# Kernel optimization log

Measured on AMD Instinct MI355X. Metric: run time of the kernel, lower is better.

## Reference

```python
import jax, jax.numpy as jnp
import numpy as np

N_P, N_D, N_S = 100000, 1000, 5000      # patients, drugs, diseases
C, H, L = 64, 4, 2                       # hidden, heads, layers
DH = C // H                              # head dim
IN_P, IN_D, IN_S = 64, 128, 64           # raw feature dims per node type
E_PD, E_DP, E_DS, E_PS = 300000, 300000, 100000, 100000
EPS = 1e-16


def setup_inputs() -> dict:
    key = jax.random.key(0)
    ks = jax.random.split(key, 20)

    def lin(k, fin, fout, prefix=()):
        return jax.random.normal(k, prefix + (fin, fout), jnp.float32) / np.sqrt(fin).astype(np.float32)

    def edges(k, e, n_src, n_dst):
        k1, k2 = jax.random.split(k)
        return jnp.stack([jax.random.randint(k1, (e,), 0, n_src),
                          jax.random.randint(k2, (e,), 0, n_dst)]).astype(jnp.int32)

    inp = {}
    inp['x_p'] = jax.random.normal(ks[0], (N_P, IN_P), jnp.float32)
    inp['x_d'] = jax.random.normal(ks[1], (N_D, IN_D), jnp.float32)
    inp['x_s'] = jax.random.normal(ks[2], (N_S, IN_S), jnp.float32)
    inp['Win_p'] = lin(ks[3], IN_P, C); inp['bin_p'] = jnp.zeros((C,), jnp.float32)
    inp['Win_d'] = lin(ks[4], IN_D, C); inp['bin_d'] = jnp.zeros((C,), jnp.float32)
    inp['Win_s'] = lin(ks[5], IN_S, C); inp['bin_s'] = jnp.zeros((C,), jnp.float32)
    inp['Wk'] = lin(ks[6], C, C, (L, 3)); inp['bk'] = jnp.zeros((L, 3, C), jnp.float32)
    inp['Wq'] = lin(ks[7], C, C, (L, 3)); inp['bq'] = jnp.zeros((L, 3, C), jnp.float32)
    inp['Wv'] = lin(ks[8], C, C, (L, 3)); inp['bv'] = jnp.zeros((L, 3, C), jnp.float32)
    inp['Wa'] = lin(ks[9], C, C, (L, 3)); inp['ba'] = jnp.zeros((L, 3, C), jnp.float32)
    inp['a_rel'] = jax.random.normal(ks[10], (L, 4, H, DH, DH), jnp.float32) / np.sqrt(DH).astype(np.float32)
    inp['m_rel'] = jax.random.normal(ks[11], (L, 4, H, DH, DH), jnp.float32) / np.sqrt(DH).astype(np.float32)
    inp['p_rel'] = jnp.ones((L, 4, H), jnp.float32)   # PyG inits rel prior to ones
    inp['skip'] = jnp.ones((L, 3), jnp.float32)       # PyG inits skip gate to ones
    inp['ei_pd'] = edges(ks[12], E_PD, N_P, N_D)  # patient -takes-> drug
    inp['ei_dp'] = edges(ks[13], E_DP, N_D, N_P)  # drug -taken_by-> patient
    inp['ei_ds'] = edges(ks[14], E_DS, N_D, N_S)  # drug -treats-> disease
    inp['ei_ps'] = edges(ks[15], E_PS, N_P, N_S)  # patient -has-> disease
    return inp


def _hgt(x_p, x_d, x_s, Win_p, bin_p, Win_d, bin_d, Win_s, bin_s,
         Wk, bk, Wq, bq, Wv, bv, Wa, ba, a_rel, m_rel, p_rel, skip,
         ei_pd, ei_dp, ei_ds, ei_ps):
    Ns = (N_P, N_D, N_S)
    # per-node-type input projection (lin_dict)
    xs = [x_p @ Win_p + bin_p, x_d @ Win_d + bin_d, x_s @ Win_s + bin_s]
    # (src_type, dst_type, edge_index) for each relation
    edge_defs = [(0, 1, ei_pd), (1, 0, ei_dp), (1, 2, ei_ds), (0, 2, ei_ps)]
    inv_sqrt_d = np.float32(1.0 / np.sqrt(DH))

    for l in range(L):  # HGTConv layers
        k_t = [(xs[t] @ Wk[l, t] + bk[l, t]).reshape(Ns[t], H, DH) for t in range(3)]
        q_t = [(xs[t] @ Wq[l, t] + bq[l, t]).reshape(Ns[t], H, DH) for t in range(3)]
        v_t = [(xs[t] @ Wv[l, t] + bv[l, t]).reshape(Ns[t], H, DH) for t in range(3)]
        out = [jnp.zeros((Ns[t], H, DH), xs[t].dtype) for t in range(3)]
        for r, (st, dt, ei) in enumerate(edge_defs):
            src, dst = ei[0], ei[1]
            # relation-specific head-wise transforms of K and V
            k_rel = jnp.einsum('nhd,hde->nhe', k_t[st], a_rel[l, r])
            v_rel = jnp.einsum('nhd,hde->nhe', v_t[st], m_rel[l, r])
            # attention logits per edge, per head: [E, H]
            alpha = (q_t[dt][dst] * k_rel[src]).sum(-1) * (p_rel[l, r] * inv_sqrt_d)
            # segment softmax over incoming edges of each dst node (per relation)
            mx = jax.ops.segment_max(alpha, dst, num_segments=Ns[dt])
            a = jnp.exp(alpha - jax.lax.stop_gradient(mx)[dst])
            den = jax.ops.segment_sum(a, dst, num_segments=Ns[dt])
            a = a / (den[dst] + EPS)
            # attention-weighted scatter-add of messages, grouped by 'sum'
            out[dt] = out[dt] + jax.ops.segment_sum(v_rel[src] * a[:, :, None], dst, num_segments=Ns[dt])
        new_xs = []
        for t in range(3):
            o = jax.nn.gelu(out[t].reshape(Ns[t], C), approximate=False) @ Wa[l, t] + ba[l, t]
            s = jax.nn.sigmoid(skip[l, t])  # learned skip gate (in == out channels)
            new_xs.append(s * o + (1.0 - s) * xs[t])
        xs = new_xs
    # concatenate node-type outputs along node axis: [N_P+N_D+N_S, C]
    return jnp.concatenate(xs, axis=0)


def reference(x_p, x_d, x_s, Win_p, bin_p, Win_d, bin_d, Win_s, bin_s,
              Wk, bk, Wq, bq, Wv, bv, Wa, ba, a_rel, m_rel, p_rel, skip,
              ei_pd, ei_dp, ei_ds, ei_ps):
    return _hgt(x_p, x_d, x_s, Win_p, bin_p, Win_d, bin_d, Win_s, bin_s,
                Wk, bk, Wq, bq, Wv, bv, Wa, ba, a_rel, m_rel, p_rel, skip,
                ei_pd, ei_dp, ei_ds, ei_ps)
```

## Files before the change

kernel.cpp:

```cpp
#include <hip/hip_runtime.h>
#include <cmath>

typedef unsigned short ush;
typedef __attribute__((ext_vector_type(8))) short short8;
typedef __attribute__((ext_vector_type(4))) float floatx4;

static constexpr int N_P = 100000, N_D = 1000, N_S = 5000, NT = N_P + N_D + N_S;
static constexpr int NC = 111000;
static constexpr int E_TOT = 800000;

static constexpr int NB0 = 128, NB2 = 64, NB3 = 64;
static constexpr int CH0 = (300000 + NB0 - 1) / NB0;
static constexpr int CH2 = (100000 + NB2 - 1) / NB2;
static constexpr int HB0_OFF = 0;
static constexpr int HB2_OFF = NB0 * 1000;
static constexpr int HB3_OFF = HB2_OFF + NB2 * 5000;
static constexpr int NCH0 = NB0 / 16, NCH2 = NB2 / 16;
static constexpr int CS0_OFF = 0;
static constexpr int CS2_OFF = NCH0 * 1000;
static constexpr int CS3_OFF = CS2_OFF + NCH2 * 5000;
static constexpr int NHIST = NB0 + NB2 + NB3;
static constexpr int NBLK_R1 = (300000 + 255) / 256;
static constexpr int NZB = (100000 + 255) / 256;

__device__ __forceinline__ float b2f(ush b) { return __uint_as_float(((unsigned)b) << 16); }
__device__ __forceinline__ ush f2b(float f) {
    unsigned u = __float_as_uint(f);
    return (ush)((u + 0x7FFFu + ((u >> 16) & 1u)) >> 16);
}

__global__ __launch_bounds__(256) void detect_kernel(const ush* __restrict__ xp,
                                                     int* __restrict__ flag) {
    __shared__ int s;
    if (threadIdx.x == 0) s = 0;
    __syncthreads();
    int c = 0;
    for (int i = threadIdx.x; i < 16384; i += 256) {
        ush h = xp[i];
        if ((h & 0x7F80) == 0x7F80) c = 1;
    }
    if (c) atomicOr(&s, 1);
    __syncthreads();
    if (threadIdx.x == 0) *flag = s;
}

static constexpr size_t OFF_WINP = 0;
static constexpr size_t OFF_BINP = 4096;
static constexpr size_t OFF_WIND = 4160;
static constexpr size_t OFF_BIND = 12352;
static constexpr size_t OFF_WINS = 12416;
static constexpr size_t OFF_BINS = 16512;
static constexpr size_t OFF_WK = 16576;
static constexpr size_t OFF_BK = 41152;
static constexpr size_t OFF_WQ = 41536;
static constexpr size_t OFF_BQ = 66112;
static constexpr size_t OFF_WV = 66496;
static constexpr size_t OFF_BV = 91072;
static constexpr size_t OFF_WA = 91456;
static constexpr size_t OFF_BA = 116032;
static constexpr size_t OFF_AREL = 116416;
static constexpr size_t OFF_MREL = 124608;
static constexpr size_t OFF_PREL = 132800;
static constexpr size_t OFF_SKIP = 132832;
static constexpr size_t CW_TOTAL = 132838;
static constexpr int NCONVB = (int)((CW_TOTAL + 255) / 256);

struct ConvArgs {
    const void* src[18];
    long cum[19];
};

__global__ __launch_bounds__(256) void convert_kernel(ConvArgs a, ush* __restrict__ dst,
                                                      int* __restrict__ cnt_r1,
                                                      const int* __restrict__ flag) {
    const int b = blockIdx.x;
    if (b >= NCONVB) {
        int g = (b - NCONVB) * 256 + threadIdx.x;
        if (g < 100000) cnt_r1[g] = 0;
        return;
    }
    const int f = *flag;
    long g = (long)b * 256 + threadIdx.x;
    if (g >= (long)CW_TOTAL) return;
    int t = 0;
    while (g >= a.cum[t + 1]) t++;
    long i = g - a.cum[t];
    float v = f ? ((const float*)a.src[t])[i] : b2f(((const ush*)a.src[t])[i]);
    dst[g] = f2b(v);
}

struct CsrB {
    const int* ei[3];
    const int* ei1;
};

__device__ __forceinline__ void hist_geom(int b, const CsrB& c, int& r, const int*& ei, int& E,
                                          int& ndst, int& e0, int& e1, int& hb) {
    if (b < NB0) {
        r = 0; ei = c.ei[0]; E = 300000; ndst = 1000;
        e0 = b * CH0; hb = HB0_OFF + b * 1000;
    } else if (b < NB0 + NB2) {
        r = 1; ei = c.ei[1]; E = 100000; ndst = 5000;
        e0 = (b - NB0) * CH2; hb = HB2_OFF + (b - NB0) * 5000;
    } else {
        r = 2; ei = c.ei[2]; E = 100000; ndst = 5000;
        e0 = (b - NB0 - NB2) * CH2; hb = HB3_OFF + (b - NB0 - NB2) * 5000;
    }
    e1 = min(E, e0 + ((r == 0) ? CH0 : CH2));
}

__global__ __launch_bounds__(256) void count_kernel(CsrB c, int* __restrict__ HB,
                                                    int* __restrict__ cnt) {
    const int b = blockIdx.x;
    if (b >= NHIST) {
        int g = (b - NHIST) * 256 + threadIdx.x;
        if (g < 300000) atomicAdd(&cnt[1000 + c.ei1[300000 + g]], 1);
        return;
    }
    __shared__ int h[5000];
    int r, E, ndst, e0, e1, hb;
    const int* ei;
    hist_geom(b, c, r, ei, E, ndst, e0, e1, hb);
    for (int d = threadIdx.x; d < ndst; d += 256) h[d] = 0;
    __syncthreads();
    for (int e = e0 + threadIdx.x; e < e1; e += 256) atomicAdd(&h[ei[E + e]], 1);
    __syncthreads();
    for (int d = threadIdx.x; d < ndst; d += 256) HB[hb + d] = h[d];
}

__device__ __forceinline__ bool cs_geom(int g, int& idx0, int& step) {
    if (g >= 48000) return false;
    if (g < 8000) {
        int c = g / 1000, d = g % 1000;
        idx0 = HB0_OFF + c * 16 * 1000 + d; step = 1000;
    } else if (g < 28000) {
        int gg = g - 8000, c = gg / 5000, d = gg % 5000;
        idx0 = HB2_OFF + c * 16 * 5000 + d; step = 5000;
    } else {
        int gg = g - 28000, c = gg / 5000, d = gg % 5000;
        idx0 = HB3_OFF + c * 16 * 5000 + d; step = 5000;
    }
    return true;
}

__global__ __launch_bounds__(256) void sumHB_kernel(const int* __restrict__ HB,
                                                    int* __restrict__ CS) {
    int g = blockIdx.x * 256 + threadIdx.x;
    int idx0, step;
    if (!cs_geom(g, idx0, step)) return;
    int s = 0;
#pragma unroll
    for (int b = 0; b < 16; b++) s += HB[idx0 + b * step];
    CS[g] = s;
}

__global__ __launch_bounds__(256) void scanCS_kernel(int* __restrict__ CS,
                                                     int* __restrict__ cnt) {
    int d = blockIdx.x * 256 + threadIdx.x;
    if (d >= 11000) return;
    int ld, nch, cs0, step, roff;
    if (d < 1000) { ld = d; nch = NCH0; cs0 = CS0_OFF + ld; step = 1000; roff = 0; }
    else if (d < 6000) { ld = d - 1000; nch = NCH2; cs0 = CS2_OFF + ld; step = 5000; roff = 101000; }
    else { ld = d - 6000; nch = NCH2; cs0 = CS3_OFF + ld; step = 5000; roff = 106000; }
    int run = 0;
    for (int c = 0; c < nch; c++) {
        int t = CS[cs0 + c * step];
        CS[cs0 + c * step] = run;
        run += t;
    }
    cnt[roff + ld] = run;
}

__global__ __launch_bounds__(256) void fixHB_kernel(int* __restrict__ HB,
                                                    const int* __restrict__ CS) {
    int g = blockIdx.x * 256 + threadIdx.x;
    int idx0, step;
    if (!cs_geom(g, idx0, step)) return;
    int run = CS[g];
#pragma unroll
    for (int b = 0; b < 16; b++) {
        int t = HB[idx0 + b * step];
        HB[idx0 + b * step] = run;
        run += t;
    }
}

__global__ __launch_bounds__(256) void scanA_kernel(const int* __restrict__ cnt,
                                                    int* __restrict__ tmp,
                                                    int* __restrict__ part) {
    __shared__ int ls[256];
    const int t = threadIdx.x;
    const int base = blockIdx.x * 1024 + t * 4;
    int v[4];
#pragma unroll
    for (int j = 0; j < 4; j++) v[j] = (base + j < NC) ? cnt[base + j] : 0;
    int tsum = v[0] + v[1] + v[2] + v[3];
    ls[t] = tsum;
    __syncthreads();
    for (int off = 1; off < 256; off <<= 1) {
        int y = (t >= off) ? ls[t - off] : 0;
        __syncthreads();
        ls[t] += y;
        __syncthreads();
    }
    int run = ls[t] - tsum;
#pragma unroll
    for (int j = 0; j < 4; j++) {
        if (base + j < NC) tmp[base + j] = run;
        run += v[j];
    }
    if (t == 255) part[blockIdx.x] = ls[255];
}

__global__ __launch_bounds__(256) void scanB_kernel(int* __restrict__ part, int nb) {
    __shared__ int ls[256];
    const int t = threadIdx.x;
    int x = (t < nb) ? part[t] : 0;
    ls[t] = x;
    __syncthreads();
    for (int off = 1; off < 256; off <<= 1) {
        int y = (t >= off) ? ls[t - off] : 0;
        __syncthreads();
        ls[t] += y;
        __syncthreads();
    }
    if (t < nb) part[t] = ls[t] - x;
    if (t == nb - 1) part[nb] = ls[t];
}

static constexpr int NSCB = (NC + 1 + 255) / 256;
__global__ __launch_bounds__(256) void scanC_kernel(const int* __restrict__ tmp,
                                                    const int* __restrict__ part,
                                                    int* __restrict__ rowptr,
                                                    int* __restrict__ cnt_r1) {
    const int b = blockIdx.x;
    if (b >= NSCB) {
        int g = (b - NSCB) * 256 + threadIdx.x;
        if (g < 100000) cnt_r1[g] = 0;
        return;
    }
    int i = b * 256 + threadIdx.x;
    if (i > NC) return;
    rowptr[i] = (i == NC) ? part[(NC + 1023) / 1024] : tmp[i] + part[i >> 10];
}

__global__ __launch_bounds__(256) void fill_kernel(CsrB c, const int* __restrict__ HB,
                                                   const int* __restrict__ rowptr,
                                                   int* __restrict__ fillpos,
                                                   int* __restrict__ col) {
    const int b = blockIdx.x;
    if (b >= NHIST) {
        int g = (b - NHIST) * 256 + threadIdx.x;
        if (g < 300000) {
            int gi = 1000 + c.ei1[300000 + g];
            int slot = rowptr[gi] + atomicAdd(&fillpos[gi], 1);
            col[slot] = c.ei1[g];
        }
        return;
    }
    __shared__ int h[5000];
    int r, E, ndst, e0, e1, hb;
    const int* ei;
    hist_geom(b, c, r, ei, E, ndst, e0, e1, hb);
    const int roff = (r == 0) ? 0 : (r == 1) ? 101000 : 106000;
    for (int d = threadIdx.x; d < ndst; d += 256) h[d] = rowptr[roff + d] + HB[hb + d];
    __syncthreads();
    for (int e = e0 + threadIdx.x; e < e1; e += 256) {
        int d = ei[E + e];
        int slot = atomicAdd(&h[d], 1);
        col[slot] = ei[e];
    }
}

__global__ __launch_bounds__(256) void eff_kernel(const ush* __restrict__ CW,
                                                  ush* __restrict__ weff) {
    const int b = blockIdx.x;
    const int l = b >> 2, r = b & 3;
    const int st_of[4] = {0, 1, 1, 0};
    const int st = st_of[r];
    ush* out = weff + (size_t)b * 8320;
    for (int idx = threadIdx.x; idx < 8320; idx += 256) {
        int n, k;
        if (idx < 8192) { k = idx >> 7; n = idx & 127; }
        else { k = -1; n = idx - 8192; }
        int kv = n >= 64;
        int j = n & 63, h = j >> 4, e = j & 15;
        const ush* W = CW + (kv ? OFF_WV : OFF_WK) + (size_t)(l * 3 + st) * 4096;
        const ush* B = CW + (kv ? OFF_BV : OFF_BK) + (size_t)(l * 3 + st) * 64;
        const ush* R = CW + (kv ? OFF_MREL : OFF_AREL) + (size_t)(l * 4 + r) * 1024;
        float acc = 0.f;
        if (k >= 0) {
#pragma unroll
            for (int d = 0; d < 16; d++)
                acc += b2f(W[k * 64 + h * 16 + d]) * b2f(R[h * 256 + d * 16 + e]);
        } else {
#pragma unroll
            for (int d = 0; d < 16; d++)
                acc += b2f(B[h * 16 + d]) * b2f(R[h * 256 + d * 16 + e]);
        }
        out[idx] = f2b(acc);
    }
}

template <int K>
__device__ __forceinline__ void stage_A(short* sA, const ush* __restrict__ X, int M, int row0) {
    for (int cid = threadIdx.x; cid < 64 * K / 8; cid += 256) {
        int r = cid / (K / 8), c0 = (cid % (K / 8)) * 8;
        int row = row0 + r;
        short8 v = {0, 0, 0, 0, 0, 0, 0, 0};
        if (row < M) v = *(const short8*)(const void*)(X + (size_t)row * K + c0);
        *(short8*)(&sA[r * (K + 8) + c0]) = v;
    }
}

template <int K>
__device__ __forceinline__ void stage_A_raw(short* sA, const void* __restrict__ X, int f,
                                            int M, int row0) {
    for (int cid = threadIdx.x; cid < 64 * K / 8; cid += 256) {
        int r = cid / (K / 8), c0 = (cid % (K / 8)) * 8;
        int row = row0 + r;
        short8 v = {0, 0, 0, 0, 0, 0, 0, 0};
        if (row < M) {
            if (f) {
// ... 32 lines not shown
#pragma unroll
    for (int c = 0; c < NOUT / 16; c++) {
        float bv = b2f(Bb[16 * c + (l & 15)]);
        acc[c] = (floatx4){bv, bv, bv, bv};
    }
#pragma unroll
    for (int s = 0; s < K / 32; s++) {
        short8 a = *(const short8*)(&sA[(16 * w + (l & 15)) * (K + 8) + 32 * s + ((l >> 4) << 3)]);
#pragma unroll
        for (int c = 0; c < NOUT / 16; c++) {
            short8 b = *(const short8*)(&sB[(s * (NOUT / 16) + c) * 512 + l * 8]);
            acc[c] = __builtin_amdgcn_mfma_f32_16x16x32_bf16(a, b, acc[c], 0, 0, 0);
        }
    }
#pragma unroll
    for (int c = 0; c < NOUT / 16; c++)
#pragma unroll
        for (int r = 0; r < 4; r++) {
            int row = row0 + 16 * w + ((l >> 4) << 2) + r;
            if (row < M) Y[(size_t)row * NOUT + 16 * c + (l & 15)] = f2b(acc[c][r]);
        }
}

struct InArgs {
    const void* raw[3];
    const ush* W[3];
    const ush* Bb[3];
    ush* X;
    const int* flag;
};

__global__ __launch_bounds__(256) void inproj_kernel(InArgs a) {
    extern __shared__ short smem[];
    const int b = blockIdx.x;
    const int f = *a.flag;
    if (b < 1563) {
        short* sA = smem;
        short* sB = smem + 64 * 72;
        stage_A_raw<64>(sA, a.raw[0], f, N_P, b * 64);
        gemm_core<64, 64>(sA, sB, a.W[0], a.Bb[0], a.X, N_P, b * 64);
    } else if (b < 1579) {
        short* sA = smem;
        short* sB = smem + 64 * 136;
        stage_A_raw<128>(sA, a.raw[1], f, N_D, (b - 1563) * 64);
        gemm_core<128, 64>(sA, sB, a.W[1], a.Bb[1], a.X + (size_t)N_P * 64, N_D,
                           (b - 1563) * 64);
    } else {
        short* sA = smem;
        short* sB = smem + 64 * 72;
        stage_A_raw<64>(sA, a.raw[2], f, N_S, (b - 1579) * 64);
        gemm_core<64, 64>(sA, sB, a.W[2], a.Bb[2], a.X + (size_t)(N_P + N_D) * 64, N_S,
                          (b - 1579) * 64);
    }
}

struct QKVArgs {
    const ush* X;
    ush* Q;
    const ush* Wq[3];
    const ush* Bq[3];
    const ush* Xr[4];
    ush* Y[4];
    const ush* Wkv[4];
    const ush* Bkv[4];
};

__global__ __launch_bounds__(256) void qkv_kernel(QKVArgs a) {
    extern __shared__ short smem[];
    short* sA = smem;
    short* sB = smem + 64 * 72;
    const int b = blockIdx.x;
    if (b < 1658) {
        int t, lb, M;
        size_t noff;
        if (b < 1563) { t = 0; lb = b; M = N_P; noff = 0; }
        else if (b < 1579) { t = 1; lb = b - 1563; M = N_D; noff = (size_t)N_P; }
        else { t = 2; lb = b - 1579; M = N_S; noff = (size_t)(N_P + N_D); }
        stage_A<64>(sA, a.X + noff * 64, M, lb * 64);
        gemm_core<64, 64>(sA, sB, a.Wq[t], a.Bq[t], a.Q + noff * 64, M, lb * 64);
    } else {
        int bb = b - 1658;
        int r, lb, M;
        if (bb < 1563) { r = 0; lb = bb; M = N_P; }
        else if (bb < 1579) { r = 1; lb = bb - 1563; M = N_D; }
        else if (bb < 1595) { r = 2; lb = bb - 1579; M = N_D; }
        else { r = 3; lb = bb - 1595; M = N_P; }
        stage_A<64>(sA, a.Xr[r], M, lb * 64);
        gemm_core<64, 128>(sA, sB, a.Wkv[r], a.Bkv[r], a.Y[r], M, lb * 64);
    }
}

struct AggrArgs {
    const int* rowptr;
    const int* col;
    const ush* KV[4];
    const ush* Q;
    const ush* prel;
    float* OUT;
};

template <int LANES>
__device__ __forceinline__ void seg_attn(const AggrArgs& a, int rel, int g, int h, int lane,
                                         const float* qf, float* o) {
    const int s0 = a.rowptr[g], s1 = a.rowptr[g + 1];
    const ush* KV = a.KV[rel];
    const float ps = b2f(a.prel[rel * 4 + h]) * 0.25f;
    float m = -1e30f, s = 0.f;
    float acc[16];
#pragma unroll
    for (int i = 0; i < 16; i++) acc[i] = 0.f;
    for (int j = s0 + lane; j < s1; j += LANES) {
        int src = a.col[j];
        const ush* kp = KV + (size_t)src * 128 + h * 16;
        short8 k0 = *(const short8*)(const void*)kp;
        short8 k1 = *(const short8*)(const void*)(kp + 8);
        short8 v0 = *(const short8*)(const void*)(kp + 64);
        short8 v1 = *(const short8*)(const void*)(kp + 72);
        float dot = 0.f;
#pragma unroll
        for (int i = 0; i < 8; i++) dot += qf[i] * b2f((ush)k0[i]);
#pragma unroll
// ... 26 lines not shown
#pragma unroll
    for (int i = 0; i < 16; i++) o[i] += acc[i] * inv;
}

template <int LANES>
__device__ __forceinline__ void job_run(const AggrArgs& a, int wid, int nd, int rel, int roff,
                                        size_t xoff, int rel2, int roff2) {
    const int lane = wid % LANES;
    const int grp = wid / LANES;
    const int d = grp >> 2, h = grp & 3;
    if (d >= nd) return;
    const ush* qp = a.Q + xoff + (size_t)d * 64 + h * 16;
    short8 q0 = *(const short8*)(const void*)qp;
    short8 q1 = *(const short8*)(const void*)(qp + 8);
    float qf[16];
#pragma unroll
    for (int i = 0; i < 8; i++) { qf[i] = b2f((ush)q0[i]); qf[8 + i] = b2f((ush)q1[i]); }
    float o[16];
#pragma unroll
    for (int i = 0; i < 16; i++) o[i] = 0.f;
    seg_attn<LANES>(a, rel, roff + d, h, lane, qf, o);
    if (rel2 >= 0) seg_attn<LANES>(a, rel2, roff2 + d, h, lane, qf, o);
    if (lane == 0) {
        float* op = a.OUT + xoff + (size_t)d * 64 + h * 16;
#pragma unroll
        for (int i = 0; i < 4; i++)
            *(floatx4*)(op + 4 * i) =
                (floatx4){o[4 * i], o[4 * i + 1], o[4 * i + 2], o[4 * i + 3]};
    }
}

__global__ __launch_bounds__(256) void aggr_kernel(AggrArgs a) {
    const int b = blockIdx.x, t = threadIdx.x;
    if (b < 250) {
        job_run<16>(a, b * 256 + t, N_D, 0, 0, (size_t)N_P * 64, -1, 0);
    } else if (b < 563) {
        job_run<4>(a, (b - 250) * 256 + t, N_S, 2, 101000, (size_t)(N_P + N_D) * 64, 3, 106000);
    } else {
        job_run<2>(a, (b - 563) * 256 + t, N_P, 1, 1000, 0, -1, 0);
    }
}

struct EpiArgs {
    const float* O;
    ush* X;
    const ush* W[3];
    const ush* Bb[3];
    const ush* skipv;
    void* fout;
    const int* flag;
    int last;
};

__global__ __launch_bounds__(256) void epi_kernel(EpiArgs a) {
    const int b = blockIdx.x;
    int t, lb, M;
    size_t noff;
    if (b < 1563) { t = 0; lb = b; M = N_P; noff = 0; }
    else if (b < 1579) { t = 1; lb = b - 1563; M = N_D; noff = (size_t)N_P; }
    else { t = 2; lb = b - 1579; M = N_S; noff = (size_t)(N_P + N_D); }
    const float* O = a.O + noff * 64;
    ush* X = a.X + noff * 64;
    const ush* W = a.W[t];
    __shared__ short sA[64 * 72];
    __shared__ short sB[8 * 512];
    const int tid = threadIdx.x;
    const int row0 = lb * 64;
    for (int cid = tid; cid < 512; cid += 256) {
        int r = cid >> 3, c0 = (cid & 7) * 8;
        int row = row0 + r;
        short8 sv = {0, 0, 0, 0, 0, 0, 0, 0};
        if (row < M) {
#pragma unroll
            for (int j = 0; j < 8; j++) {
                float v = O[(size_t)row * 64 + c0 + j];
                sv[j] = (short)f2b(0.5f * v * (1.0f + erff(v * 0.70710678118654752f)));
            }
        }
        *(short8*)(&sA[r * 72 + c0]) = sv;
    }
    __syncthreads();
    const float sg = 1.f / (1.f + expf(-b2f(a.skipv[t])));
    for (int u = tid; u < 512; u += 256) {
        int f = u >> 6, l = u & 63;
        int s = f >> 2, c = f & 3;
        int kbase = 32 * s + ((l >> 4) << 3), n = 16 * c + (l & 15);
        short8 v;
#pragma unroll
        for (int j = 0; j < 8; j++) v[j] = (short)W[(size_t)(kbase + j) * 64 + n];
        *(short8*)(&sB[f * 512 + l * 8]) = v;
    }
    __syncthreads();
    const int w = tid >> 6, l = tid & 63;
    floatx4 acc[4];
#pragma unroll
    for (int c = 0; c < 4; c++) {
        float bv = b2f(a.Bb[t][16 * c + (l & 15)]);
        acc[c] = (floatx4){bv, bv, bv, bv};
    }
#pragma unroll
    for (int s = 0; s < 2; s++) {
        short8 av = *(const short8*)(&sA[(16 * w + (l & 15)) * 72 + 32 * s + ((l >> 4) << 3)]);
#pragma unroll
        for (int c = 0; c < 4; c++) {
            short8 bv = *(const short8*)(&sB[(s * 4 + c) * 512 + l * 8]);
            acc[c] = __builtin_amdgcn_mfma_f32_16x16x32_bf16(av, bv, acc[c], 0, 0, 0);
        }
    }
    const int fl = a.last ? *a.flag : 0;
#pragma unroll
    for (int c = 0; c < 4; c++)
#pragma unroll
        for (int r = 0; r < 4; r++) {
            int row = row0 + 16 * w + ((l >> 4) << 2) + r;
            if (row >= M) continue;
            size_t off = (size_t)row * 64 + 16 * c + (l & 15);
            float val = sg * acc[c][r] + (1.f - sg) * b2f(X[off]);
            if (!a.last) {
                X[off] = f2b(val);
            } else {
                size_t goff = (noff + row) * 64 + 16 * c + (l & 15);
                if (fl)
                    ((float*)a.fout)[goff] = val;
                else
                    ((ush*)a.fout)[goff] = f2b(val);
            }
        }
}

extern "C" void kernel_launch(void* const* d_in, const int* in_sizes, int n_in,
                              void* d_out, int out_size, void* d_ws, size_t ws_size,
                              hipStream_t stream) {
    char* w = (char*)d_ws;
    int* FLAG = (int*)w;    w += 64;
    ush* CW = (ush*)w;      w += ((CW_TOTAL * 2 + 63) / 64) * 64;
    ush* WEFFB = (ush*)w;   w += ((size_t)8 * 8320 * 2 + 63) / 64 * 64;
    ush* X = (ush*)w;       w += (size_t)NT * 64 * 2;
    ush* Q = (ush*)w;       w += (size_t)NT * 64 * 2;
    ush* KV0 = (ush*)w;     w += (size_t)N_P * 128 * 2;
    ush* KV1 = (ush*)w;     w += (size_t)N_D * 128 * 2;
    ush* KV2 = (ush*)w;     w += (size_t)N_D * 128 * 2;
    ush* KV3 = (ush*)w;     w += (size_t)N_P * 128 * 2;
    float* OUT = (float*)w; w += (size_t)NT * 64 * 4;
    int* CNT = (int*)w;     w += (size_t)NC * 4;
    int* TMP = (int*)w;     w += (size_t)NC * 4;
    int* PART = (int*)w;    w += 512;
    int* ROWPTR = (int*)w;  w += (size_t)(NC + 1) * 4;
    int* COL = (int*)w;     w += (size_t)E_TOT * 4;
    int* HB = (int*)OUT;
    int* CS = (int*)OUT + 800000;

    detect_kernel<<<1, 256, 0, stream>>>((const ush*)d_in[0], FLAG);
    static const long sz[18] = {4096, 64, 8192, 64, 4096, 64, 24576, 384, 24576, 384,
                                24576, 384, 24576, 384, 8192, 8192, 32, 6};
    ConvArgs ca;
    long cum = 0;
    for (int t = 0; t < 18; t++) {
        ca.src[t] = d_in[3 + t];
        ca.cum[t] = cum;
        cum += sz[t];
    }
    ca.cum[18] = cum;
    convert_kernel<<<NCONVB + NZB, 256, 0, stream>>>(ca, CW, CNT + 1000, FLAG);

    CsrB cb;
    cb.ei[0] = (const int*)d_in[21];
    cb.ei[1] = (const int*)d_in[23];
    cb.ei[2] = (const int*)d_in[24];
    cb.ei1 = (const int*)d_in[22];
    count_kernel<<<NHIST + NBLK_R1, 256, 0, stream>>>(cb, HB, CNT);
    sumHB_kernel<<<(48000 + 255) / 256, 256, 0, stream>>>(HB, CS);
    scanCS_kernel<<<(11000 + 255) / 256, 256, 0, stream>>>(CS, CNT);
    scanA_kernel<<<(NC + 1023) / 1024, 256, 0, stream>>>(CNT, TMP, PART);
    scanB_kernel<<<1, 256, 0, stream>>>(PART, (NC + 1023) / 1024);
    scanC_kernel<<<NSCB + NZB, 256, 0, stream>>>(TMP, PART, ROWPTR, CNT + 1000);
    fixHB_kernel<<<(48000 + 255) / 256, 256, 0, stream>>>(HB, CS);
    fill_kernel<<<NHIST + NBLK_R1, 256, 0, stream>>>(cb, HB, ROWPTR, CNT, COL);

    eff_kernel<<<8, 256, 0, stream>>>(CW, WEFFB);

    const size_t toff[3] = {0, (size_t)N_P, (size_t)(N_P + N_D)};

    InArgs ia;
    ia.raw[0] = d_in[0];
    ia.raw[1] = d_in[1];
    ia.raw[2] = d_in[2];
    ia.W[0] = CW + OFF_WINP; ia.Bb[0] = CW + OFF_BINP;
    ia.W[1] = CW + OFF_WIND; ia.Bb[1] = CW + OFF_BIND;
    ia.W[2] = CW + OFF_WINS; ia.Bb[2] = CW + OFF_BINS;
    ia.X = X;
    ia.flag = FLAG;
    inproj_kernel<<<1658, 256, 33792, stream>>>(ia);

    for (int l = 0; l < 2; l++) {
        QKVArgs qk;
        qk.X = X;
        qk.Q = Q;
        ush* KVr[4] = {KV0, KV1, KV2, KV3};
        const int rst[4] = {0, 1, 1, 0};
        for (int t = 0; t < 3; t++) {
            qk.Wq[t] = CW + OFF_WQ + (size_t)(l * 3 + t) * 4096;
            qk.Bq[t] = CW + OFF_BQ + (l * 3 + t) * 64;
        }
        for (int r = 0; r < 4; r++) {
            qk.Xr[r] = X + toff[rst[r]] * 64;
            qk.Y[r] = KVr[r];
            const ush* we = WEFFB + (size_t)(l * 4 + r) * 8320;
            qk.Wkv[r] = we;
            qk.Bkv[r] = we + 8192;
        }
        qkv_kernel<<<4816, 256, 25600, stream>>>(qk);

        AggrArgs aa;
        aa.rowptr = ROWPTR;
        aa.col = COL;
        for (int r = 0; r < 4; r++) aa.KV[r] = KVr[r];
        aa.Q = Q;
        aa.prel = CW + OFF_PREL + l * 16;
        aa.OUT = OUT;
        aggr_kernel<<<3688, 256, 0, stream>>>(aa);

        EpiArgs ea;
        ea.O = OUT;
        ea.X = X;
        for (int t = 0; t < 3; t++) {
            ea.W[t] = CW + OFF_WA + (size_t)(l * 3 + t) * 4096;
            ea.Bb[t] = CW + OFF_BA + (l * 3 + t) * 64;
        }
        ea.skipv = CW + OFF_SKIP + l * 3;
        ea.fout = d_out;
        ea.flag = FLAG;
        ea.last = (l == 1) ? 1 : 0;
        epi_kernel<<<1658, 256, 0, stream>>>(ea);
    }
}
```

Measured before the change: 393.6 us.

## Fuse CSR build, projections and QKV into fewer launches; apply GELU in aggregation

Collapses the many small CSR-construction, scan, weight-conversion and projection kernels into four combined launches, and overlaps CSR fill with the first-layer QKV GEMM. QKV now reads each node tile once and produces Q plus both relation K/V outputs from it. GELU moves from the epilogue into the aggregation store, so the intermediate is written as bf16 instead of fp32. The runtime dtype-detect kernel is replaced by host-side checks on input sizes. The main costs targeted are launch overhead, repeated activation reads and intermediate traffic; the price is larger shared memory per block and more branching inside the merged kernels.

```diff
diff --git a/kernel.cpp b/kernel.cpp
--- a/kernel.cpp
+++ b/kernel.cpp
@@ -27,21 +27,6 @@
 __device__ __forceinline__ ush f2b(float f) {
     unsigned u = __float_as_uint(f);
     return (ush)((u + 0x7FFFu + ((u >> 16) & 1u)) >> 16);
-}
-
-__global__ __launch_bounds__(256) void detect_kernel(const ush* __restrict__ xp,
-                                                     int* __restrict__ flag) {
-    __shared__ int s;
-    if (threadIdx.x == 0) s = 0;
-    __syncthreads();
-    int c = 0;
-    for (int i = threadIdx.x; i < 16384; i += 256) {
-        ush h = xp[i];
-        if ((h & 0x7F80) == 0x7F80) c = 1;
-    }
-    if (c) atomicOr(&s, 1);
-    __syncthreads();
-    if (threadIdx.x == 0) *flag = s;
 }
 
 static constexpr size_t OFF_WINP = 0;
@@ -64,30 +49,13 @@
 static constexpr size_t OFF_SKIP = 132832;
 static constexpr size_t CW_TOTAL = 132838;
 static constexpr int NCONVB = (int)((CW_TOTAL + 255) / 256);
+static constexpr int NSCB = (NC + 1 + 255) / 256;
 
 struct ConvArgs {
     const void* src[18];
     long cum[19];
+    int fl[18];
 };
-
-__global__ __launch_bounds__(256) void convert_kernel(ConvArgs a, ush* __restrict__ dst,
-                                                      int* __restrict__ cnt_r1,
-                                                      const int* __restrict__ flag) {
-    const int b = blockIdx.x;
-    if (b >= NCONVB) {
-        int g = (b - NCONVB) * 256 + threadIdx.x;
-        if (g < 100000) cnt_r1[g] = 0;
-        return;
-    }
-    const int f = *flag;
-    long g = (long)b * 256 + threadIdx.x;
-    if (g >= (long)CW_TOTAL) return;
-    int t = 0;
-    while (g >= a.cum[t + 1]) t++;
-    long i = g - a.cum[t];
-    float v = f ? ((const float*)a.src[t])[i] : b2f(((const ush*)a.src[t])[i]);
-    dst[g] = f2b(v);
-}
 
 struct CsrB {
     const int* ei[3];
@@ -109,25 +77,6 @@
     e1 = min(E, e0 + ((r == 0) ? CH0 : CH2));
 }
 
-__global__ __launch_bounds__(256) void count_kernel(CsrB c, int* __restrict__ HB,
-                                                    int* __restrict__ cnt) {
-    const int b = blockIdx.x;
-    if (b >= NHIST) {
-        int g = (b - NHIST) * 256 + threadIdx.x;
-        if (g < 300000) atomicAdd(&cnt[1000 + c.ei1[300000 + g]], 1);
-        return;
-    }
-    __shared__ int h[5000];
-    int r, E, ndst, e0, e1, hb;
-    const int* ei;
-    hist_geom(b, c, r, ei, E, ndst, e0, e1, hb);
-    for (int d = threadIdx.x; d < ndst; d += 256) h[d] = 0;
-    __syncthreads();
-    for (int e = e0 + threadIdx.x; e < e1; e += 256) atomicAdd(&h[ei[E + e]], 1);
-    __syncthreads();
-    for (int d = threadIdx.x; d < ndst; d += 256) HB[hb + d] = h[d];
-}
-
 __device__ __forceinline__ bool cs_geom(int g, int& idx0, int& step) {
     if (g >= 48000) return false;
     if (g < 8000) {
@@ -143,162 +92,31 @@
     return true;
 }
 
-__global__ __launch_bounds__(256) void sumHB_kernel(const int* __restrict__ HB,
-                                                    int* __restrict__ CS) {
-    int g = blockIdx.x * 256 + threadIdx.x;
-    int idx0, step;
-    if (!cs_geom(g, idx0, step)) return;
-    int s = 0;
-#pragma unroll
-    for (int b = 0; b < 16; b++) s += HB[idx0 + b * step];
-    CS[g] = s;
-}
-
-__global__ __launch_bounds__(256) void scanCS_kernel(int* __restrict__ CS,
-                                                     int* __restrict__ cnt) {
-    int d = blockIdx.x * 256 + threadIdx.x;
-    if (d >= 11000) return;
-    int ld, nch, cs0, step, roff;
-    if (d < 1000) { ld = d; nch = NCH0; cs0 = CS0_OFF + ld; step = 1000; roff = 0; }
-    else if (d < 6000) { ld = d - 1000; nch = NCH2; cs0 = CS2_OFF + ld; step = 5000; roff = 101000; }
-    else { ld = d - 6000; nch = NCH2; cs0 = CS3_OFF + ld; step = 5000; roff = 106000; }
-    int run = 0;
-    for (int c = 0; c < nch; c++) {
-        int t = CS[cs0 + c * step];
-        CS[cs0 + c * step] = run;
-        run += t;
-    }
-    cnt[roff + ld] = run;
-}
-
-__global__ __launch_bounds__(256) void fixHB_kernel(int* __restrict__ HB,
-                                                    const int* __restrict__ CS) {
-    int g = blockIdx.x * 256 + threadIdx.x;
-    int idx0, step;
-    if (!cs_geom(g, idx0, step)) return;
-    int run = CS[g];
-#pragma unroll
-    for (int b = 0; b < 16; b++) {
-        int t = HB[idx0 + b * step];
-        HB[idx0 + b * step] = run;
-        run += t;
-    }
-}
-
-__global__ __launch_bounds__(256) void scanA_kernel(const int* __restrict__ cnt,
-                                                    int* __restrict__ tmp,
-                                                    int* __restrict__ part) {
-    __shared__ int ls[256];
-    const int t = threadIdx.x;
-    const int base = blockIdx.x * 1024 + t * 4;
-    int v[4];
-#pragma unroll
-    for (int j = 0; j < 4; j++) v[j] = (base + j < NC) ? cnt[base + j] : 0;
-    int tsum = v[0] + v[1] + v[2] + v[3];
-    ls[t] = tsum;
-    __syncthreads();
-    for (int off = 1; off < 256; off <<= 1) {
-        int y = (t >= off) ? ls[t - off] : 0;
+__global__ __launch_bounds__(256) void k1_kernel(ConvArgs a, ush* __restrict__ dst,
+                                                 int* __restrict__ cnt_r1, CsrB c,
+                                                 int* __restrict__ HB) {
+    const int b = blockIdx.x;
+    if (b < NCONVB) {
+        long g = (long)b * 256 + threadIdx.x;
+        if (g >= (long)CW_TOTAL) return;
+        int t = 0;
+        while (g >= a.cum[t + 1]) t++;
+        long i = g - a.cum[t];
+        float v = a.fl[t] ? ((const float*)a.src[t])[i] : b2f(((const ush*)a.src[t])[i]);
+        dst[g] = f2b(v);
+    } else if (b < NCONVB + NZB) {
+        int g = (b - NCONVB) * 256 + threadIdx.x;
+        if (g < 100000) cnt_r1[g] = 0;
+    } else {
+        __shared__ int h[5000];
+        int r, E, ndst, e0, e1, hb;
+        const int* ei;
+        hist_geom(b - NCONVB - NZB, c, r, ei, E, ndst, e0, e1, hb);
+        for (int d = threadIdx.x; d < ndst; d += 256) h[d] = 0;
         __syncthreads();
-        ls[t] += y;
+        for (int e = e0 + threadIdx.x; e < e1; e += 256) atomicAdd(&h[ei[E + e]], 1);
         __syncthreads();
-    }
-    int run = ls[t] - tsum;
-#pragma unroll
-    for (int j = 0; j < 4; j++) {
-        if (base + j < NC) tmp[base + j] = run;
-        run += v[j];
-    }
-    if (t == 255) part[blockIdx.x] = ls[255];
-}
-
-__global__ __launch_bounds__(256) void scanB_kernel(int* __restrict__ part, int nb) {
-    __shared__ int ls[256];
-    const int t = threadIdx.x;
-    int x = (t < nb) ? part[t] : 0;
-    ls[t] = x;
-    __syncthreads();
-    for (int off = 1; off < 256; off <<= 1) {
-        int y = (t >= off) ? ls[t - off] : 0;
-        __syncthreads();
-        ls[t] += y;
-        __syncthreads();
-    }
-    if (t < nb) part[t] = ls[t] - x;
-    if (t == nb - 1) part[nb] = ls[t];
-}
-
-static constexpr int NSCB = (NC + 1 + 255) / 256;
-__global__ __launch_bounds__(256) void scanC_kernel(const int* __restrict__ tmp,
-                                                    const int* __restrict__ part,
-                                                    int* __restrict__ rowptr,
-                                                    int* __restrict__ cnt_r1) {
-    const int b = blockIdx.x;
-    if (b >= NSCB) {
-        int g = (b - NSCB) * 256 + threadIdx.x;
-        if (g < 100000) cnt_r1[g] = 0;
-        return;
-    }
-    int i = b * 256 + threadIdx.x;
-    if (i > NC) return;
-    rowptr[i] = (i == NC) ? part[(NC + 1023) / 1024] : tmp[i] + part[i >> 10];
-}
-
-__global__ __launch_bounds__(256) void fill_kernel(CsrB c, const int* __restrict__ HB,
-                                                   const int* __restrict__ rowptr,
-                                                   int* __restrict__ fillpos,
-                                                   int* __restrict__ col) {
-    const int b = blockIdx.x;
-    if (b >= NHIST) {
-        int g = (b - NHIST) * 256 + threadIdx.x;
-        if (g < 300000) {
-            int gi = 1000 + c.ei1[300000 + g];
-            int slot = rowptr[gi] + atomicAdd(&fillpos[gi], 1);
-            col[slot] = c.ei1[g];
-        }
-        return;
-    }
-    __shared__ int h[5000];
-    int r, E, ndst, e0, e1, hb;
-    const int* ei;
-    hist_geom(b, c, r, ei, E, ndst, e0, e1, hb);
-    const int roff = (r == 0) ? 0 : (r == 1) ? 101000 : 106000;
-    for (int d = threadIdx.x; d < ndst; d += 256) h[d] = rowptr[roff + d] + HB[hb + d];
-    __syncthreads();
-    for (int e = e0 + threadIdx.x; e < e1; e += 256) {
-        int d = ei[E + e];
-        int slot = atomicAdd(&h[d], 1);
-        col[slot] = ei[e];
-    }
-}
-
-__global__ __launch_bounds__(256) void eff_kernel(const ush* __restrict__ CW,
-                                                  ush* __restrict__ weff) {
-    const int b = blockIdx.x;
-    const int l = b >> 2, r = b & 3;
-    const int st_of[4] = {0, 1, 1, 0};
-    const int st = st_of[r];
-    ush* out = weff + (size_t)b * 8320;
-    for (int idx = threadIdx.x; idx < 8320; idx += 256) {
-        int n, k;
-        if (idx < 8192) { k = idx >> 7; n = idx & 127; }
-        else { k = -1; n = idx - 8192; }
-        int kv = n >= 64;
-        int j = n & 63, h = j >> 4, e = j & 15;
-        const ush* W = CW + (kv ? OFF_WV : OFF_WK) + (size_t)(l * 3 + st) * 4096;
-        const ush* B = CW + (kv ? OFF_BV : OFF_BK) + (size_t)(l * 3 + st) * 64;
-        const ush* R = CW + (kv ? OFF_MREL : OFF_AREL) + (size_t)(l * 4 + r) * 1024;
-        float acc = 0.f;
-        if (k >= 0) {
-#pragma unroll
-            for (int d = 0; d < 16; d++)
-                acc += b2f(W[k * 64 + h * 16 + d]) * b2f(R[h * 256 + d * 16 + e]);
-        } else {
-#pragma unroll
-            for (int d = 0; d < 16; d++)
-                acc += b2f(B[h * 16 + d]) * b2f(R[h * 256 + d * 16 + e]);
-        }
-        out[idx] = f2b(acc);
+        for (int d = threadIdx.x; d < ndst; d += 256) HB[hb + d] = h[d];
     }
 }
 
@@ -377,71 +195,270 @@
         }
 }
 
-struct InArgs {
+template <int NG>
+__device__ __forceinline__ void gemm_wide(const short* sA, short* sB,
+                                          const ush* __restrict__ Wq, const ush* __restrict__ Bq,
+                                          ush* __restrict__ Yq,
+                                          const ush* __restrict__ WeA, ush* __restrict__ YA,
+                                          const ush* __restrict__ WeB, ush* __restrict__ YB,
+                                          int M, int row0) {
+    constexpr int NF = 2 * NG;
+    const int tid = threadIdx.x;
+    for (int u = tid; u < NF * 64; u += 256) {
+        int f = u >> 6, l = u & 63;
+        int s = f / NG, c = f % NG;
+        int kbase = 32 * s + ((l >> 4) << 3);
+        const ush* W; int ld, cw;
+        if (c < 4) { W = Wq; ld = 64; cw = 16 * c; }
+        else if (c < 12) { W = WeA; ld = 128; cw = 16 * (c - 4); }
+        else { W = WeB; ld = 128; cw = 16 * (c - 12); }
+        int n = cw + (l & 15);
+        short8 v;
+#pragma unroll
+        for (int j = 0; j < 8; j++) v[j] = (short)W[(size_t)(kbase + j) * ld + n];
+        *(short8*)(&sB[f * 512 + l * 8]) = v;
+    }
+    __syncthreads();
+    const int w = tid >> 6, l = tid & 63;
+    floatx4 acc[NG];
+#pragma unroll
+    for (int c = 0; c < NG; c++) {
+        float bv;
+        if (c < 4) bv = b2f(Bq[16 * c + (l & 15)]);
+        else if (c < 12) bv = b2f(WeA[8192 + 16 * (c - 4) + (l & 15)]);
+        else bv = b2f(WeB[8192 + 16 * (c - 12) + (l & 15)]);
+        acc[c] = (floatx4){bv, bv, bv, bv};
+    }
+#pragma unroll
+    for (int s = 0; s < 2; s++) {
+        short8 a = *(const short8*)(&sA[(16 * w + (l & 15)) * 72 + 32 * s + ((l >> 4) << 3)]);
+#pragma unroll
+        for (int c = 0; c < NG; c++) {
+            short8 b = *(const short8*)(&sB[(s * NG + c) * 512 + l * 8]);
+            acc[c] = __builtin_amdgcn_mfma_f32_16x16x32_bf16(a, b, acc[c], 0, 0, 0);
+        }
+    }
+#pragma unroll
+    for (int c = 0; c < NG; c++)
+#pragma unroll
+        for (int r = 0; r < 4; r++) {
+            int row = row0 + 16 * w + ((l >> 4) << 2) + r;
+            if (row >= M) continue;
+            ush val = f2b(acc[c][r]);
+            if (c < 4) Yq[(size_t)row * 64 + 16 * c + (l & 15)] = val;
+            else if (c < 12) YA[(size_t)row * 128 + 16 * (c - 4) + (l & 15)] = val;
+            else YB[(size_t)row * 128 + 16 * (c - 12) + (l & 15)] = val;
+        }
+}
+
+struct K2Args {
     const void* raw[3];
+    int f[3];
     const ush* W[3];
     const ush* Bb[3];
     ush* X;
-    const int* flag;
+    const int* HB;
+    int* CS;
+    int* cnt;
+    const int* ei1;
 };
 
-__global__ __launch_bounds__(256) void inproj_kernel(InArgs a) {
+__global__ __launch_bounds__(256) void k2_kernel(K2Args a) {
     extern __shared__ short smem[];
     const int b = blockIdx.x;
-    const int f = *a.flag;
-    if (b < 1563) {
-        short* sA = smem;
-        short* sB = smem + 64 * 72;
-        stage_A_raw<64>(sA, a.raw[0], f, N_P, b * 64);
-        gemm_core<64, 64>(sA, sB, a.W[0], a.Bb[0], a.X, N_P, b * 64);
-    } else if (b < 1579) {
-        short* sA = smem;
-        short* sB = smem + 64 * 136;
-        stage_A_raw<128>(sA, a.raw[1], f, N_D, (b - 1563) * 64);
-        gemm_core<128, 64>(sA, sB, a.W[1], a.Bb[1], a.X + (size_t)N_P * 64, N_D,
-                           (b - 1563) * 64);
+    if (b < 1658) {
+        if (b < 1563) {
+            short* sA = smem; short* sB = smem + 64 * 72;
+            stage_A_raw<64>(sA, a.raw[0], a.f[0], N_P, b * 64);
+            gemm_core<64, 64>(sA, sB, a.W[0], a.Bb[0], a.X, N_P, b * 64);
+        } else if (b < 1579) {
+            short* sA = smem; short* sB = smem + 64 * 136;
+            stage_A_raw<128>(sA, a.raw[1], a.f[1], N_D, (b - 1563) * 64);
+            gemm_core<128, 64>(sA, sB, a.W[1], a.Bb[1], a.X + (size_t)N_P * 64, N_D,
+                               (b - 1563) * 64);
+        } else {
+            short* sA = smem; short* sB = smem + 64 * 72;
+            stage_A_raw<64>(sA, a.raw[2], a.f[2], N_S, (b - 1579) * 64);
+            gemm_core<64, 64>(sA, sB, a.W[2], a.Bb[2], a.X + (size_t)(N_P + N_D) * 64, N_S,
+                              (b - 1579) * 64);
+        }
+    } else if (b < 1701) {
+        int d = (b - 1658) * 256 + threadIdx.x;
+        if (d >= 11000) return;
+        int ld_, nch, base, step, cs0, csstep, roff;
+        if (d < 1000) { ld_ = d; nch = NCH0; base = HB0_OFF + ld_; step = 1000;
+                        cs0 = CS0_OFF + ld_; csstep = 1000; roff = 0; }
+        else if (d < 6000) { ld_ = d - 1000; nch = NCH2; base = HB2_OFF + ld_; step = 5000;
+                             cs0 = CS2_OFF + ld_; csstep = 5000; roff = 101000; }
+        else { ld_ = d - 6000; nch = NCH2; base = HB3_OFF + ld_; step = 5000;
+               cs0 = CS3_OFF + ld_; csstep = 5000; roff = 106000; }
+        int run = 0;
+        for (int cc = 0; cc < nch; cc++) {
+            int s = 0;
+#pragma unroll
+            for (int bb = 0; bb < 16; bb++) s += a.HB[base + (cc * 16 + bb) * step];
+            a.CS[cs0 + cc * csstep] = run;
+            run += s;
+        }
+        a.cnt[roff + ld_] = run;
     } else {
-        short* sA = smem;
-        short* sB = smem + 64 * 72;
-        stage_A_raw<64>(sA, a.raw[2], f, N_S, (b - 1579) * 64);
-        gemm_core<64, 64>(sA, sB, a.W[2], a.Bb[2], a.X + (size_t)(N_P + N_D) * 64, N_S,
-                          (b - 1579) * 64);
+        int g = (b - 1701) * 256 + threadIdx.x;
+        if (g < 300000) atomicAdd(&a.cnt[1000 + a.ei1[300000 + g]], 1);
+    }
+}
+
+__global__ __launch_bounds__(256) void k3_kernel(const int* __restrict__ cnt,
+                                                 int* __restrict__ tmp,
+                                                 int* __restrict__ part,
+                                                 const ush* __restrict__ CW,
+                                                 ush* __restrict__ weff) {
+    const int b = blockIdx.x;
+    if (b < 109) {
+        __shared__ int ls[256];
+        const int t = threadIdx.x;
+        const int base = b * 1024 + t * 4;
+        int v[4];
+#pragma unroll
+        for (int j = 0; j < 4; j++) v[j] = (base + j < NC) ? cnt[base + j] : 0;
+        int tsum = v[0] + v[1] + v[2] + v[3];
+        ls[t] = tsum;
+        __syncthreads();
+        for (int off = 1; off < 256; off <<= 1) {
+            int y = (t >= off) ? ls[t - off] : 0;
+            __syncthreads();
+            ls[t] += y;
+            __syncthreads();
+        }
+        int run = ls[t] - tsum;
+#pragma unroll
+        for (int j = 0; j < 4; j++) {
+            if (base + j < NC) tmp[base + j] = run;
+            run += v[j];
+        }
+        if (t == 255) part[b] = ls[255];
+    } else {
+        const int eb = b - 109;
+        const int l = eb >> 2, r = eb & 3;
+        const int st_of[4] = {0, 1, 1, 0};
+        const int st = st_of[r];
+        ush* out = weff + (size_t)eb * 8320;
+        for (int idx = threadIdx.x; idx < 8320; idx += 256) {
+            int n, k;
+            if (idx < 8192) { k = idx >> 7; n = idx & 127; }
+            else { k = -1; n = idx - 8192; }
+            int kv = n >= 64;
+            int j = n & 63, h = j >> 4, e = j & 15;
+            const ush* W = CW + (kv ? OFF_WV : OFF_WK) + (size_t)(l * 3 + st) * 4096;
+            const ush* B = CW + (kv ? OFF_BV : OFF_BK) + (size_t)(l * 3 + st) * 64;
+            const ush* R = CW + (kv ? OFF_MREL : OFF_AREL) + (size_t)(l * 4 + r) * 1024;
+            float acc = 0.f;
+            if (k >= 0) {
+#pragma unroll
+                for (int d = 0; d < 16; d++)
+                    acc += b2f(W[k * 64 + h * 16 + d]) * b2f(R[h * 256 + d * 16 + e]);
+            } else {
+#pragma unroll
+                for (int d = 0; d < 16; d++)
+                    acc += b2f(B[h * 16 + d]) * b2f(R[h * 256 + d * 16 + e]);
+            }
+            out[idx] = f2b(acc);
+        }
+    }
+}
+
+__global__ __launch_bounds__(256) void k4_kernel(const int* __restrict__ tmp,
+                                                 const int* __restrict__ part,
+                                                 int* __restrict__ rowptr,
+                                                 int* __restrict__ HB,
+                                                 const int* __restrict__ CS,
+                                                 int* __restrict__ fillpos) {
+    const int b = blockIdx.x;
+    if (b < NSCB) {
+        __shared__ int ls[256];
+        const int t = threadIdx.x;
+        ls[t] = (t < 109) ? part[t] : 0;
+        __syncthreads();
+        for (int off = 1; off < 256; off <<= 1) {
+            int y = (t >= off) ? ls[t - off] : 0;
+            __syncthreads();
+            ls[t] += y;
+            __syncthreads();
+        }
+        int i = b * 256 + t;
+        if (i <= NC)
+            rowptr[i] = (i == NC) ? ls[255] : tmp[i] + ((i >> 10) ? ls[(i >> 10) - 1] : 0);
+    } else if (b < NSCB + 188) {
+        int g = (b - NSCB) * 256 + threadIdx.x;
+        int idx0, step;
+        if (!cs_geom(g, idx0, step)) return;
+        int run = CS[g];
+#pragma unroll
+        for (int bb = 0; bb < 16; bb++) {
+            int t2 = HB[idx0 + bb * step];
+            HB[idx0 + bb * step] = run;
+            run += t2;
+        }
+    } else {
+        int g = (b - NSCB - 188) * 256 + threadIdx.x;
+        if (g < 100000) fillpos[g] = 0;
     }
 }
 
 struct QKVArgs {
     const ush* X;
     ush* Q;
+    ush* KV[4];
     const ush* Wq[3];
     const ush* Bq[3];
-    const ush* Xr[4];
-    ush* Y[4];
-    const ush* Wkv[4];
-    const ush* Bkv[4];
+    const ush* We[4];
+    CsrB cb;
+    const int* HB;
+    const int* rowptr;
+    int* fillpos;
+    int* col;
 };
 
-__global__ __launch_bounds__(256) void qkv_kernel(QKVArgs a) {
+__global__ __launch_bounds__(256) void qkvfill_kernel(QKVArgs a) {
     extern __shared__ short smem[];
-    short* sA = smem;
-    short* sB = smem + 64 * 72;
     const int b = blockIdx.x;
     if (b < 1658) {
-        int t, lb, M;
-        size_t noff;
-        if (b < 1563) { t = 0; lb = b; M = N_P; noff = 0; }
-        else if (b < 1579) { t = 1; lb = b - 1563; M = N_D; noff = (size_t)N_P; }
-        else { t = 2; lb = b - 1579; M = N_S; noff = (size_t)(N_P + N_D); }
-        stage_A<64>(sA, a.X + noff * 64, M, lb * 64);
-        gemm_core<64, 64>(sA, sB, a.Wq[t], a.Bq[t], a.Q + noff * 64, M, lb * 64);
+        short* sA = smem;
+        short* sB = smem + 64 * 72;
+        if (b < 1563) {
+            stage_A<64>(sA, a.X, N_P, b * 64);
+            gemm_wide<20>(sA, sB, a.Wq[0], a.Bq[0], a.Q, a.We[0], a.KV[0], a.We[3], a.KV[3],
+                          N_P, b * 64);
+        } else if (b < 1579) {
+            int lb = b - 1563;
+            stage_A<64>(sA, a.X + (size_t)N_P * 64, N_D, lb * 64);
+            gemm_wide<20>(sA, sB, a.Wq[1], a.Bq[1], a.Q + (size_t)N_P * 64, a.We[1], a.KV[1],
+                          a.We[2], a.KV[2], N_D, lb * 64);
+        } else {
+            int lb = b - 1579;
+            stage_A<64>(sA, a.X + (size_t)(N_P + N_D) * 64, N_S, lb * 64);
+            gemm_wide<4>(sA, sB, a.Wq[2], a.Bq[2], a.Q + (size_t)(N_P + N_D) * 64,
+                         nullptr, nullptr, nullptr, nullptr, N_S, lb * 64);
+        }
+    } else if (b < 1658 + NHIST) {
+        int* h = (int*)smem;
+        int r, E, ndst, e0, e1, hb;
+        const int* ei;
+        hist_geom(b - 1658, a.cb, r, ei, E, ndst, e0, e1, hb);
+        const int roff = (r == 0) ? 0 : (r == 1) ? 101000 : 106000;
+        for (int d = threadIdx.x; d < ndst; d += 256) h[d] = a.rowptr[roff + d] + a.HB[hb + d];
+        __syncthreads();
+        for (int e = e0 + threadIdx.x; e < e1; e += 256) {
+            int d = ei[E + e];
+            int slot = atomicAdd(&h[d], 1);
+            a.col[slot] = ei[e];
+        }
     } else {
-        int bb = b - 1658;
-        int r, lb, M;
-        if (bb < 1563) { r = 0; lb = bb; M = N_P; }
-        else if (bb < 1579) { r = 1; lb = bb - 1563; M = N_D; }
-        else if (bb < 1595) { r = 2; lb = bb - 1579; M = N_D; }
-        else { r = 3; lb = bb - 1595; M = N_P; }
-        stage_A<64>(sA, a.Xr[r], M, lb * 64);
-        gemm_core<64, 128>(sA, sB, a.Wkv[r], a.Bkv[r], a.Y[r], M, lb * 64);
+        int g = (b - 1658 - NHIST) * 256 + threadIdx.x;
+        if (g < 300000) {
+            int gi = 1000 + a.cb.ei1[300000 + g];
+            int slot = a.rowptr[gi] + atomicAdd(&a.fillpos[gi], 1);
+            a.col[slot] = a.cb.ei1[g];
+        }
     }
 }
 
@@ -451,7 +468,7 @@
     const ush* KV[4];
     const ush* Q;
     const ush* prel;
-    float* OUT;
+    ush* OUT;
 };
 
 template <int LANES>
@@ -524,11 +541,17 @@
     seg_attn<LANES>(a, rel, roff + d, h, lane, qf, o);
     if (rel2 >= 0) seg_attn<LANES>(a, rel2, roff2 + d, h, lane, qf, o);
     if (lane == 0) {
-        float* op = a.OUT + xoff + (size_t)d * 64 + h * 16;
-#pragma unroll
-        for (int i = 0; i < 4; i++)
-            *(floatx4*)(op + 4 * i) =
-                (floatx4){o[4 * i], o[4 * i + 1], o[4 * i + 2], o[4 * i + 3]};
+        ush* op = a.OUT + xoff + (size_t)d * 64 + h * 16;
+        short8 w0, w1;
+#pragma unroll
+        for (int i = 0; i < 8; i++) {
+            float va = o[i];
+            w0[i] = (short)f2b(0.5f * va * (1.0f + erff(va * 0.70710678118654752f)));
+            float vb = o[8 + i];
+            w1[i] = (short)f2b(0.5f * vb * (1.0f + erff(vb * 0.70710678118654752f)));
+        }
+        *(short8*)(op) = w0;
+        *(short8*)(op + 8) = w1;
     }
 }
 
@@ -544,13 +567,13 @@
 }
 
 struct EpiArgs {
-    const float* O;
+    const ush* O;
     ush* X;
     const ush* W[3];
     const ush* Bb[3];
     const ush* skipv;
     void* fout;
-    const int* flag;
+    int foutf;
     int last;
 };
 
@@ -561,7 +584,7 @@
     if (b < 1563) { t = 0; lb = b; M = N_P; noff = 0; }
     else if (b < 1579) { t = 1; lb = b - 1563; M = N_D; noff = (size_t)N_P; }
     else { t = 2; lb = b - 1579; M = N_S; noff = (size_t)(N_P + N_D); }
-    const float* O = a.O + noff * 64;
+    const ush* O = a.O + noff * 64;
     ush* X = a.X + noff * 64;
     const ush* W = a.W[t];
     __shared__ short sA[64 * 72];
@@ -572,13 +595,7 @@
         int r = cid >> 3, c0 = (cid & 7) * 8;
         int row = row0 + r;
         short8 sv = {0, 0, 0, 0, 0, 0, 0, 0};
-        if (row < M) {
-#pragma unroll
-            for (int j = 0; j < 8; j++) {
-                float v = O[(size_t)row * 64 + c0 + j];
-                sv[j] = (short)f2b(0.5f * v * (1.0f + erff(v * 0.70710678118654752f)));
-            }
-        }
+        if (row < M) sv = *(const short8*)(const void*)(O + (size_t)row * 64 + c0);
         *(short8*)(&sA[r * 72 + c0]) = sv;
     }
     __syncthreads();
@@ -609,7 +626,6 @@
             acc[c] = __builtin_amdgcn_mfma_f32_16x16x32_bf16(av, bv, acc[c], 0, 0, 0);
         }
     }
-    const int fl = a.last ? *a.flag : 0;
 #pragma unroll
     for (int c = 0; c < 4; c++)
 #pragma unroll
@@ -622,7 +638,7 @@
                 X[off] = f2b(val);
             } else {
                 size_t goff = (noff + row) * 64 + 16 * c + (l & 15);
-                if (fl)
+                if (a.foutf)
                     ((float*)a.fout)[goff] = val;
                 else
                     ((ush*)a.fout)[goff] = f2b(val);
@@ -634,7 +650,7 @@
                               void* d_out, int out_size, void* d_ws, size_t ws_size,
                               hipStream_t stream) {
     char* w = (char*)d_ws;
-    int* FLAG = (int*)w;    w += 64;
+    w += 64;
     ush* CW = (ush*)w;      w += ((CW_TOTAL * 2 + 63) / 64) * 64;
     ush* WEFFB = (ush*)w;   w += ((size_t)8 * 8320 * 2 + 63) / 64 * 64;
     ush* X = (ush*)w;       w += (size_t)NT * 64 * 2;
@@ -643,7 +659,7 @@
     ush* KV1 = (ush*)w;     w += (size_t)N_D * 128 * 2;
     ush* KV2 = (ush*)w;     w += (size_t)N_D * 128 * 2;
     ush* KV3 = (ush*)w;     w += (size_t)N_P * 128 * 2;
-    float* OUT = (float*)w; w += (size_t)NT * 64 * 4;
+    ush* OUT = (ush*)w;     w += (size_t)NT * 64 * 4;
     int* CNT = (int*)w;     w += (size_t)NC * 4;
     int* TMP = (int*)w;     w += (size_t)NC * 4;
     int* PART = (int*)w;    w += 512;
@@ -652,7 +668,6 @@
     int* HB = (int*)OUT;
     int* CS = (int*)OUT + 800000;
 
-    detect_kernel<<<1, 256, 0, stream>>>((const ush*)d_in[0], FLAG);
     static const long sz[18] = {4096, 64, 8192, 64, 4096, 64, 24576, 384, 24576, 384,
                                 24576, 384, 24576, 384, 8192, 8192, 32, 6};
     ConvArgs ca;
@@ -660,58 +675,56 @@
     for (int t = 0; t < 18; t++) {
         ca.src[t] = d_in[3 + t];
         ca.cum[t] = cum;
+        ca.fl[t] = (in_sizes[3 + t] != (int)(sz[t] * 2)) ? 1 : 0;
         cum += sz[t];
     }
     ca.cum[18] = cum;
-    convert_kernel<<<NCONVB + NZB, 256, 0, stream>>>(ca, CW, CNT + 1000, FLAG);
 
     CsrB cb;
     cb.ei[0] = (const int*)d_in[21];
     cb.ei[1] = (const int*)d_in[23];
     cb.ei[2] = (const int*)d_in[24];
     cb.ei1 = (const int*)d_in[22];
-    count_kernel<<<NHIST + NBLK_R1, 256, 0, stream>>>(cb, HB, CNT);
-    sumHB_kernel<<<(48000 + 255) / 256, 256, 0, stream>>>(HB, CS);
-    scanCS_kernel<<<(11000 + 255) / 256, 256, 0, stream>>>(CS, CNT);
-    scanA_kernel<<<(NC + 1023) / 1024, 256, 0, stream>>>(CNT, TMP, PART);
-    scanB_kernel<<<1, 256, 0, stream>>>(PART, (NC + 1023) / 1024);
-    scanC_kernel<<<NSCB + NZB, 256, 0, stream>>>(TMP, PART, ROWPTR, CNT + 1000);
-    fixHB_kernel<<<(48000 + 255) / 256, 256, 0, stream>>>(HB, CS);
-    fill_kernel<<<NHIST + NBLK_R1, 256, 0, stream>>>(cb, HB, ROWPTR, CNT, COL);
-
-    eff_kernel<<<8, 256, 0, stream>>>(CW, WEFFB);
-
-    const size_t toff[3] = {0, (size_t)N_P, (size_t)(N_P + N_D)};
-
-    InArgs ia;
-    ia.raw[0] = d_in[0];
-    ia.raw[1] = d_in[1];
-    ia.raw[2] = d_in[2];
-    ia.W[0] = CW + OFF_WINP; ia.Bb[0] = CW + OFF_BINP;
-    ia.W[1] = CW + OFF_WIND; ia.Bb[1] = CW + OFF_BIND;
-    ia.W[2] = CW + OFF_WINS; ia.Bb[2] = CW + OFF_BINS;
-    ia.X = X;
-    ia.flag = FLAG;
-    inproj_kernel<<<1658, 256, 33792, stream>>>(ia);
+
+    k1_kernel<<<NCONVB + NZB + NHIST, 256, 0, stream>>>(ca, CW, CNT + 1000, cb, HB);
+
+    K2Args k2;
+    k2.raw[0] = d_in[0]; k2.f[0] = (in_sizes[0] != N_P * 64 * 2) ? 1 : 0;
+    k2.raw[1] = d_in[1]; k2.f[1] = (in_sizes[1] != N_D * 128 * 2) ? 1 : 0;
+    k2.raw[2] = d_in[2]; k2.f[2] = (in_sizes[2] != N_S * 64 * 2) ? 1 : 0;
+    k2.W[0] = CW + OFF_WINP; k2.Bb[0] = CW + OFF_BINP;
+    k2.W[1] = CW + OFF_WIND; k2.Bb[1] = CW + OFF_BIND;
+    k2.W[2] = CW + OFF_WINS; k2.Bb[2] = CW + OFF_BINS;
+    k2.X = X;
+    k2.HB = HB; k2.CS = CS; k2.cnt = CNT; k2.ei1 = cb.ei1;
+    k2_kernel<<<1701 + NBLK_R1, 256, 33792, stream>>>(k2);
+
+    k3_kernel<<<109 + 8, 256, 0, stream>>>(CNT, TMP, PART, CW, WEFFB);
+
+    k4_kernel<<<NSCB + 188 + NZB, 256, 0, stream>>>(TMP, PART, ROWPTR, HB, CS, CNT + 1000);
+
+    ush* KVr[4] = {KV0, KV1, KV2, KV3};
+    const int foutf = (out_size != NT * 64 * 2) ? 1 : 0;
 
     for (int l = 0; l < 2; l++) {
         QKVArgs qk;
         qk.X = X;
         qk.Q = Q;
-        ush* KVr[4] = {KV0, KV1, KV2, KV3};
-        const int rst[4] = {0, 1, 1, 0};
+        for (int r = 0; r < 4; r++) {
+            qk.KV[r] = KVr[r];
+            qk.We[r] = WEFFB + (size_t)(l * 4 + r) * 8320;
+        }
         for (int t = 0; t < 3; t++) {
             qk.Wq[t] = CW + OFF_WQ + (size_t)(l * 3 + t) * 4096;
             qk.Bq[t] = CW + OFF_BQ + (l * 3 + t) * 64;
         }
-        for (int r = 0; r < 4; r++) {
-            qk.Xr[r] = X + toff[rst[r]] * 64;
-            qk.Y[r] = KVr[r];
-            const ush* we = WEFFB + (size_t)(l * 4 + r) * 8320;
-            qk.Wkv[r] = we;
-            qk.Bkv[r] = we + 8192;
-        }
-        qkv_kernel<<<4816, 256, 25600, stream>>>(qk);
+        qk.cb = cb;
+        qk.HB = HB;
+        qk.rowptr = ROWPTR;
+        qk.fillpos = CNT;
+        qk.col = COL;
+        const int qgrid = (l == 0) ? (1658 + NHIST + NBLK_R1) : 1658;
+        qkvfill_kernel<<<qgrid, 256, 50176, stream>>>(qk);
 
         AggrArgs aa;
         aa.rowptr = ROWPTR;
@@ -731,7 +744,7 @@
         }
         ea.skipv = CW + OFF_SKIP + l * 3;
         ea.fout = d_out;
-        ea.flag = FLAG;
+        ea.foutf = foutf;
         ea.last = (l == 1) ? 1 : 0;
         epi_kernel<<<1658, 256, 0, stream>>>(ea);
     }
```

Result: faster. 369.3 us (-6.2%).
